# Optimization experiments

Measured on AMD Instinct MI355X. Metric: run time of the kernel, lower is better.

## Reference

```python
import jax, jax.numpy as jnp
import numpy as np

B, N, T, F_IN = 16, 1024, 12, 1
D_MODEL, D_K, D_V, H, K = 512, 32, 32, 3, 3
C = 32  # nb_chev_filter == nb_time_filter


def _ln(x, g, b, eps=1e-5):
    mu = jnp.mean(x, -1, keepdims=True)
    var = jnp.var(x, -1, keepdims=True)
    return (x - mu) * jax.lax.rsqrt(var + eps) * g + b


def _conv(x, w, b):
    y = jax.lax.conv_general_dilated(x, w, (1, 1), 'VALID',
                                     dimension_numbers=('NCHW', 'OIHW', 'NCHW'))
    return y + b[None, :, None, None]


def setup_inputs() -> dict:
    key = jax.random.key(0)
    ks = iter(jax.random.split(key, 40))
    rn = lambda s, sc=0.02: jax.random.normal(next(ks), s, jnp.float32) * sc
    return dict(
        x=rn((B, N, F_IN, T), 1.0),
        res_att=rn((B, F_IN, H, T, T), 0.1),
        pos_embed_T=rn((T, N)),
        gamma_T=jnp.ones((N,)), beta_T=jnp.zeros((N,)),
        WQ_t=rn((N, D_K * H)), WK_t=rn((N, D_K * H)), WV_t=rn((N, D_V * H)),
        fc_t=rn((H * D_V, N)),
        pre_conv_w=rn((D_MODEL, T, 1, F_IN)), pre_conv_b=rn((D_MODEL,)),
        pos_embed_S=rn((N, D_MODEL)),
        gamma_S=jnp.ones((D_MODEL,)), beta_S=jnp.zeros((D_MODEL,)),
        WQ_s=rn((D_MODEL, D_K * K)), WK_s=rn((D_MODEL, D_K * K)),
        cheb_polys=rn((K, N, N), 0.05),
        adj_pa=(jax.random.uniform(next(ks), (N, N)) < 0.01).astype(jnp.float32),
        cheb_mask=rn((K, N, N)),
        Theta=rn((K, F_IN, C), 0.1),
        gtu3_w=rn((2 * C, C, 1, 3)), gtu3_b=rn((2 * C,)),
        gtu5_w=rn((2 * C, C, 1, 5)), gtu5_b=rn((2 * C,)),
        gtu7_w=rn((2 * C, C, 1, 7)), gtu7_b=rn((2 * C,)),
        res_conv_w=rn((C, F_IN, 1, 1)), res_conv_b=rn((C,)),
        fcmy_w=rn((3 * T - 12, T)), fcmy_b=rn((T,)),
        gamma_f=jnp.ones((C,)), beta_f=jnp.zeros((C,)),
    )


def reference(x, res_att, pos_embed_T, gamma_T, beta_T, WQ_t, WK_t, WV_t, fc_t,
              pre_conv_w, pre_conv_b, pos_embed_S, gamma_S, beta_S, WQ_s, WK_s,
              cheb_polys, adj_pa, cheb_mask, Theta,
              gtu3_w, gtu3_b, gtu5_w, gtu5_b, gtu7_w, gtu7_b,
              res_conv_w, res_conv_b, fcmy_w, fcmy_b, gamma_f, beta_f):
    B_, N_, F_, T_ = x.shape
    # ---- temporal embedding (num_of_features == 1 branch): (B,F,T,N) ----
    TEmx = _ln(jnp.transpose(x, (0, 2, 3, 1)) + pos_embed_T[None, None], gamma_T, beta_T)

    # ---- temporal MHA with residual attention bias ----
    def heads(e, W, d):
        y = e @ W  # (B,F,T,H*d)
        return jnp.transpose(y.reshape(B_, F_, T_, H, d), (0, 1, 3, 2, 4))  # (B,F,H,T,d)
    Q, Kt, V = heads(TEmx, WQ_t, D_K), heads(TEmx, WK_t, D_K), heads(TEmx, WV_t, D_V)
    re_At = jnp.einsum('bfhqd,bfhkd->bfhqk', Q, Kt) / np.sqrt(D_K) + res_att
    attn = jax.nn.softmax(re_At, axis=-1)
    ctx = jnp.einsum('bfhqk,bfhkd->bfhqd', attn, V)
    ctx = jnp.transpose(ctx, (0, 1, 3, 2, 4)).reshape(B_, F_, T_, H * D_V)
    one_n, zero_n = jnp.ones((N_,), x.dtype), jnp.zeros((N_,), x.dtype)
    TATout = _ln(ctx @ fc_t + TEmx, one_n, zero_n)  # fresh LayerNorm(d_model) -> gamma=1, beta=0

    # ---- pre_conv: Conv2d(T, d_model, kernel=(1,F)) on (B,T,N,F); take last col ----
    x_TAt = jnp.einsum('btnf,dtf->bnd', jnp.transpose(TATout, (0, 2, 3, 1)),
                       pre_conv_w[:, :, 0, :]) + pre_conv_b  # (B,N,d_model)

    # ---- spatial embedding + spatial attention scores (no softmax) ----
    SEmx = _ln(x_TAt + pos_embed_S[None], gamma_S, beta_S)  # dropout = identity (eval)
    Qs = jnp.transpose((SEmx @ WQ_s).reshape(B_, N_, K, D_K), (0, 2, 1, 3))
    Ks = jnp.transpose((SEmx @ WK_s).reshape(B_, N_, K, D_K), (0, 2, 1, 3))
    STAt = jnp.einsum('bknd,bkmd->bknm', Qs, Ks) / np.sqrt(D_K)  # (B,K,N,N)

    # ---- Chebyshev graph conv weighted by spatial attention ----
    satt = jax.nn.softmax(STAt + (adj_pa[None] * cheb_mask)[None], axis=2)
    Tka = cheb_polys[None] * satt  # (B,K,N,N)
    rhs = jnp.einsum('bkmn,bmft->bknft', Tka, x)  # T_k_with_at^T @ x over all t
    spatial_gcn = jax.nn.relu(jnp.einsum('bknft,kfo->bnot', rhs, Theta))  # (B,N,C,T)

    # ---- gated temporal convs (GTU) ----
    X = jnp.transpose(spatial_gcn, (0, 2, 1, 3))  # (B,C,N,T)
    def gtu(w, b):
        y = _conv(X, w, b)
        return jnp.tanh(y[:, :C]) * jax.nn.sigmoid(y[:, C:])
    time_conv = jnp.concatenate([gtu(gtu3_w, gtu3_b), gtu(gtu5_w, gtu5_b),
                                 gtu(gtu7_w, gtu7_b)], axis=-1)  # (B,C,N,3T-12)
    time_conv = time_conv @ fcmy_w + fcmy_b  # (B,C,N,T)
    tco = jax.nn.relu(time_conv)  # num_of_features == 1 branch

    # ---- residual 1x1 conv + final LayerNorm over channel dim ----
    x_res = _conv(jnp.transpose(x, (0, 2, 1, 3)), res_conv_w, res_conv_b)  # (B,C,N,T)
    out = _ln(jnp.transpose(jax.nn.relu(x_res + tco), (0, 3, 2, 1)), gamma_f, beta_f)
    out = jnp.transpose(out, (0, 2, 3, 1))  # (B,N,C,T)
    return out, re_At
```

## Files before the change

### kernel.cpp

```cpp
#include <hip/hip_runtime.h>
#include <hip/hip_bf16.h>
#include <math.h>

#define B_ 16
#define N_ 1024
#define T_ 12
#define DM_ 512
#define H_ 3
#define K_ 3
#define C_ 32
#define RSQRT_DK 0.17677669529663687f

typedef __attribute__((ext_vector_type(8))) short bf16x8;
typedef __attribute__((ext_vector_type(4))) float f32x4;

__device__ __forceinline__ ushort f2bf(float f) {
  uint u = __float_as_uint(f);
  return (ushort)((u + 0x7FFF + ((u >> 16) & 1)) >> 16);
}

__global__ void k1_temporal_ln(const float* __restrict__ x, const float* __restrict__ posT,
                               const float* __restrict__ gT, const float* __restrict__ bT,
                               float* __restrict__ TEmx) {
  int row = blockIdx.x;
  int b = row / T_, t = row - b * T_;
  __shared__ float red[256], red2[256];
  float v[4]; float s = 0.f, s2 = 0.f;
  for (int i = 0; i < 4; ++i) {
    int n = threadIdx.x + (i << 8);
    float val = x[(b * N_ + n) * T_ + t] + posT[t * N_ + n];
    v[i] = val; s += val; s2 += val * val;
  }
  red[threadIdx.x] = s; red2[threadIdx.x] = s2;
  __syncthreads();
  for (int off = 128; off > 0; off >>= 1) {
    if (threadIdx.x < off) { red[threadIdx.x] += red[threadIdx.x + off]; red2[threadIdx.x] += red2[threadIdx.x + off]; }
    __syncthreads();
  }
  float mu = red[0] * (1.f / N_);
  float rs = rsqrtf(red2[0] * (1.f / N_) - mu * mu + 1e-5f);
  for (int i = 0; i < 4; ++i) {
    int n = threadIdx.x + (i << 8);
    TEmx[row * N_ + n] = (v[i] - mu) * rs * gT[n] + bT[n];
  }
}

__global__ __launch_bounds__(256) void k2_qkv(const float* __restrict__ TEmx,
                       const float* __restrict__ WQ, const float* __restrict__ WK,
                       const float* __restrict__ WV, float* __restrict__ part) {
  int kc = blockIdx.x, row = blockIdx.y;
  __shared__ float e[256];
  int tid = threadIdx.x;
  e[tid] = TEmx[row * N_ + kc * 256 + tid];
  __syncthreads();
  for (int col = tid; col < 288; col += 256) {
    int which = col / 96, j = col - which * 96;
    const float* W = (which == 0) ? WQ : ((which == 1) ? WK : WV);
    const float* Wp = W + (size_t)(kc * 256) * 96 + j;
    float acc = 0.f;
    #pragma unroll 8
    for (int n = 0; n < 256; ++n) acc += e[n] * Wp[n * 96];
    part[(row * 4 + kc) * 288 + col] = acc;
  }
}

__global__ void k3a_attn(const float* __restrict__ part, const float* __restrict__ res_att,
                         float* __restrict__ reAt_out, float* __restrict__ ctx) {
  int b = blockIdx.x;
  __shared__ float q_l[T_ * 288];
  __shared__ float s_l[H_ * T_ * T_];
  for (int i = threadIdx.x; i < T_ * 288; i += 256) {
    int t = i / 288, col = i - t * 288;
    const float* pr = &part[(size_t)((b * T_ + t) * 4) * 288 + col];
    q_l[i] = pr[0] + pr[288] + pr[576] + pr[864];
  }
  __syncthreads();
  for (int idx = threadIdx.x; idx < H_ * T_ * T_; idx += 256) {
    int h = idx / 144, r = idx - h * 144, qi = r / 12, ki = r - qi * 12;
    float acc = 0.f;
    #pragma unroll
    for (int d = 0; d < 32; ++d)
      acc += q_l[qi * 288 + h * 32 + d] * q_l[ki * 288 + 96 + h * 32 + d];
    float sv = acc * RSQRT_DK + res_att[(b * H_ + h) * 144 + qi * 12 + ki];
    s_l[idx] = sv;
    reAt_out[(b * H_ + h) * 144 + qi * 12 + ki] = sv;
  }
  __syncthreads();
  if (threadIdx.x < 36) {
    int h = threadIdx.x / 12, qi = threadIdx.x - h * 12;
    float mx = -1e30f;
    for (int ki = 0; ki < 12; ++ki) mx = fmaxf(mx, s_l[h * 144 + qi * 12 + ki]);
    float sum = 0.f;
    for (int ki = 0; ki < 12; ++ki) { float p = __expf(s_l[h * 144 + qi * 12 + ki] - mx); s_l[h * 144 + qi * 12 + ki] = p; sum += p; }
    float inv = 1.f / sum;
    for (int ki = 0; ki < 12; ++ki) s_l[h * 144 + qi * 12 + ki] *= inv;
  }
  __syncthreads();
  for (int idx = threadIdx.x; idx < T_ * 96; idx += 256) {
    int qi = idx / 96, hd = idx - qi * 96, h = hd >> 5, d = hd & 31;
    float acc = 0.f;
    for (int ki = 0; ki < 12; ++ki)
      acc += s_l[h * 144 + qi * 12 + ki] * q_l[ki * 288 + 192 + h * 32 + d];
    ctx[(b * T_ + qi) * 96 + hd] = acc;
  }
}

__global__ __launch_bounds__(1024) void k3b_tat(const float* __restrict__ ctx,
                        const float* __restrict__ fc_t,
                        const float* __restrict__ TEmx, float* __restrict__ TAT) {
  int row = blockIdx.x;
  __shared__ float c_l[96];
  __shared__ float red[16], red2[16];
  int tid = threadIdx.x;
  if (tid < 96) c_l[tid] = ctx[row * 96 + tid];
  __syncthreads();
  float acc = TEmx[row * N_ + tid];
  #pragma unroll 12
  for (int j = 0; j < 96; ++j) acc = fmaf(c_l[j], fc_t[j * N_ + tid], acc);
  float s = acc, s2 = acc * acc;
  #pragma unroll
  for (int off = 32; off > 0; off >>= 1) {
    s  += __shfl_xor(s, off);
    s2 += __shfl_xor(s2, off);
  }
  int w = tid >> 6;
  if ((tid & 63) == 0) { red[w] = s; red2[w] = s2; }
  __syncthreads();
  float ts = 0.f, ts2 = 0.f;
  #pragma unroll
  for (int i = 0; i < 16; ++i) { ts += red[i]; ts2 += red2[i]; }
  float mu = ts * (1.f / N_);
  float rs = rsqrtf(ts2 * (1.f / N_) - mu * mu + 1e-5f);
  TAT[row * N_ + tid] = (acc - mu) * rs;
}

__global__ void k4_preconv_ln(const float* __restrict__ TAT, const float* __restrict__ pcw,
                              const float* __restrict__ pcb, const float* __restrict__ posS,
                              const float* __restrict__ gS, const float* __restrict__ bS,
                              float* __restrict__ SEmx) {
  int bn = blockIdx.x; int b = bn >> 10, n = bn & 1023;
  __shared__ float tc[12];
  __shared__ float red[256], red2[256];
  if (threadIdx.x < 12) tc[threadIdx.x] = TAT[(b * T_ + threadIdx.x) * N_ + n];
  __syncthreads();
  float v[2]; float s = 0.f, s2 = 0.f;
  for (int i = 0; i < 2; ++i) {
    int d = threadIdx.x + (i << 8);
    float acc = pcb[d];
    #pragma unroll
    for (int t = 0; t < 12; ++t) acc += tc[t] * pcw[d * 12 + t];
    acc += posS[n * DM_ + d];
    v[i] = acc; s += acc; s2 += acc * acc;
  }
  red[threadIdx.x] = s; red2[threadIdx.x] = s2;
  __syncthreads();
  for (int off = 128; off > 0; off >>= 1) {
    if (threadIdx.x < off) { red[threadIdx.x] += red[threadIdx.x + off]; red2[threadIdx.x] += red2[threadIdx.x + off]; }
    __syncthreads();
  }
  float mu = red[0] * (1.f / DM_);
  float rs = rsqrtf(red2[0] * (1.f / DM_) - mu * mu + 1e-5f);
  for (int i = 0; i < 2; ++i) {
    int d = threadIdx.x + (i << 8);
    SEmx[bn * DM_ + d] = (v[i] - mu) * rs * gS[d] + bS[d];
  }
}

__global__ void k5_pre(const float* __restrict__ WQs, const float* __restrict__ WKs,
                       ushort* __restrict__ wpre) {
  int idx = blockIdx.x * 256 + threadIdx.x;
  int k = idx / 192, col = idx - k * 192;
  float v = (col < 96) ? WQs[k * 96 + col] : WKs[k * 96 + (col - 96)];
  wpre[col * 512 + k] = f2bf(v);
}

__global__ __launch_bounds__(256) void k5_qks(const float* __restrict__ SEmx,
                                              const ushort* __restrict__ wpre,
                                              __hip_bfloat16* __restrict__ Qs,
                                              __hip_bfloat16* __restrict__ Ks) {
  int b = blockIdx.y, n0 = blockIdx.x * 32;
  __shared__ __align__(16) ushort SE_h[32 * 520];
  int tid = threadIdx.x;
  for (int idx = tid; idx < 4096; idx += 256) {
    int r = idx >> 7, cq = idx & 127;
    float4 v = *(const float4*)&SEmx[((size_t)((b << 10) + n0 + r)) * DM_ + cq * 4];
    uint lo = (uint)f2bf(v.x) | ((uint)f2bf(v.y) << 16);
    uint hi = (uint)f2bf(v.z) | ((uint)f2bf(v.w) << 16);
    *(uint2*)&SE_h[r * 520 + cq * 4] = make_uint2(lo, hi);
  }
  __syncthreads();

  int w = tid >> 6, lane = tid & 63, quad = lane >> 4, c16 = lane & 15;
  f32x4 acc[3][2];
  #pragma unroll
  for (int mi = 0; mi < 3; ++mi)
    #pragma unroll
    for (int nt = 0; nt < 2; ++nt) acc[mi][nt] = (f32x4){0.f, 0.f, 0.f, 0.f};

  for (int ks = 0; ks < 16; ++ks) {
    bf16x8 Bf0 = *(const bf16x8*)&SE_h[(0 * 16 + c16) * 520 + ks * 32 + quad * 8];
    bf16x8 Bf1 = *(const bf16x8*)&SE_h[(1 * 16 + c16) * 520 + ks * 32 + quad * 8];
    #pragma unroll
    for (int mi = 0; mi < 3; ++mi) {
      int m = (w * 3 + mi) * 16 + c16;
      bf16x8 Af = *(const bf16x8*)&wpre[m * 512 + ks * 32 + quad * 8];
      acc[mi][0] = __builtin_amdgcn_mfma_f32_16x16x32_bf16(Af, Bf0, acc[mi][0], 0, 0, 0);
      acc[mi][1] = __builtin_amdgcn_mfma_f32_16x16x32_bf16(Af, Bf1, acc[mi][1], 0, 0, 0);
    }
  }
  #pragma unroll
  for (int mi = 0; mi < 3; ++mi) {
    int mb = (w * 3 + mi) * 16;
    #pragma unroll
    for (int nt = 0; nt < 2; ++nt) {
      int node = n0 + nt * 16 + c16;
      #pragma unroll
      for (int r = 0; r < 4; ++r) {
        int m = mb + quad * 4 + r;
        int j = (m < 96) ? m : m - 96;
        int kk = j >> 5, dd = j & 31;
        __hip_bfloat16* o = (m < 96) ? Qs : Ks;
        o[(((b * K_ + kk) * N_) + node) * 32 + dd] = __float2bfloat16(acc[mi][nt][r]);
      }
    }
  }
}

__global__ void k6_pre(const float* __restrict__ adj, const float* __restrict__ mask,
                       const float* __restrict__ cheb, uint* __restrict__ pk) {
  int idx = blockIdx.x * 256 + threadIdx.x;
  int mn = idx & (N_ * N_ - 1);
  uint lo = f2bf(adj[mn] * mask[idx]);
  uint hi = f2bf(cheb[idx]);
  pk[idx] = lo | (hi << 16);
}

__global__ __launch_bounds__(256) void k6_spatial(
    const __hip_bfloat16* __restrict__ Qs, const __hip_bfloat16* __restrict__ Ks,
    const uint* __restrict__ pk, const float* __restrict__ x,
    float* __restrict__ rhs) {
  const int b  = blockIdx.x;
  const int k  = blockIdx.y;
  const int n0 = blockIdx.z * 32;
  const ushort* Qb = (const ushort*)(Qs + (size_t)((b * K_ + k) * N_) * 32);
  const ushort* Kb = (const ushort*)(Ks + (size_t)((b * K_ + k) * N_) * 32);
  const uint* pkk = pk + (size_t)k * (N_ * N_);
  const float* xb = x + b * N_ * T_;

  __shared__ float wmu[4][32], well[4][32];
  __shared__ float wacc[4][32][12];

  const int tid  = threadIdx.x;
  const int w    = tid >> 6, lane = tid & 63;
  const int quad = lane >> 4, c16 = lane & 15;

  bf16x8 bfr0 = *(const bf16x8*)(Kb + (size_t)(n0 + c16) * 32 + quad * 8);
  bf16x8 bfr1 = *(const bf16x8*)(Kb + (size_t)(n0 + 16 + c16) * 32 + quad * 8);

  float mu0 = -1e30f, mu1 = -1e30f, el0 = 0.f, el1 = 0.f;
  float acc0[12], acc1[12];
  #pragma unroll
  for (int t = 0; t < 12; ++t) { acc0[t] = 0.f; acc1[t] = 0.f; }

  for (int s = 0; s < 16; ++s) {
    const int m0 = s * 64 + w * 16;
    bf16x8 af = *(const bf16x8*)(Qb + (size_t)(m0 + c16) * 32 + quad * 8);
    f32x4 z = {0.f, 0.f, 0.f, 0.f};
    f32x4 sc0 = __builtin_amdgcn_mfma_f32_16x16x32_bf16(af, bfr0, z, 0, 0, 0);
    f32x4 sc1 = __builtin_amdgcn_mfma_f32_16x16x32_bf16(af, bfr1, z, 0, 0, 0);

    const int mrow = m0 + quad * 4;
    float sv0[4], sv1[4], ch0[4], ch1[4];
    #pragma unroll
    for (int r = 0; r < 4; ++r) {
      uint p2 = pkk[(size_t)(mrow + r) * N_ + n0 + c16];
      uint q2 = pkk[(size_t)(mrow + r) * N_ + n0 + 16 + c16];
      sv0[r] = sc0[r] * RSQRT_DK + __uint_as_float(p2 << 16);
      ch0[r] = __uint_as_float(p2 & 0xFFFF0000u);
      sv1[r] = sc1[r] * RSQRT_DK + __uint_as_float(q2 << 16);
      ch1[r] = __uint_as_float(q2 & 0xFFFF0000u);
    }
    float cm0 = fmaxf(fmaxf(sv0[0], sv0[1]), fmaxf(sv0[2], sv0[3]));
    float cm1 = fmaxf(fmaxf(sv1[0], sv1[1]), fmaxf(sv1[2], sv1[3]));
    cm0 = fmaxf(cm0, __shfl_xor(cm0, 16)); cm0 = fmaxf(cm0, __shfl_xor(cm0, 32));
    cm1 = fmaxf(cm1, __shfl_xor(cm1, 16)); cm1 = fmaxf(cm1, __shfl_xor(cm1, 32));
    float nm0 = fmaxf(mu0, cm0), nm1 = fmaxf(mu1, cm1);
    float f0 = __expf(mu0 - nm0), f1 = __expf(mu1 - nm1);
    mu0 = nm0; mu1 = nm1;
    el0 *= f0; el1 *= f1;
    #pragma unroll
    for (int t = 0; t < 12; ++t) { acc0[t] *= f0; acc1[t] *= f1; }

    float p0[4], p1[4];
    #pragma unroll
    for (int r = 0; r < 4; ++r) {
      p0[r] = __expf(sv0[r] - mu0); el0 += p0[r]; p0[r] *= ch0[r];
      p1[r] = __expf(sv1[r] - mu1); el1 += p1[r]; p1[r] *= ch1[r];
    }
    #pragma unroll
    for (int r = 0; r < 4; ++r) {
      const float4* xr = (const float4*)(xb + (size_t)(mrow + r) * 12);
      float4 xA = xr[0], xB = xr[1], xC = xr[2];
      float xv[12] = {xA.x, xA.y, xA.z, xA.w, xB.x, xB.y, xB.z, xB.w,
                      xC.x, xC.y, xC.z, xC.w};
      float px0 = p0[r], px1 = p1[r];
      #pragma unroll
      for (int t = 0; t < 12; ++t) {
        acc0[t] = fmaf(px0, xv[t], acc0[t]);
        acc1[t] = fmaf(px1, xv[t], acc1[t]);
      }
    }
  }

  #pragma unroll
  for (int off = 16; off <= 32; off <<= 1) {
    el0 += __shfl_xor(el0, off);
    el1 += __shfl_xor(el1, off);
    #pragma unroll
    for (int t = 0; t < 12; ++t) {
      acc0[t] += __shfl_xor(acc0[t], off);
      acc1[t] += __shfl_xor(acc1[t], off);
    }
  }
  if (quad == 0) {
    wmu[w][c16] = mu0; well[w][c16] = el0;
    #pragma unroll
    for (int t = 0; t < 12; ++t) wacc[w][c16][t] = acc0[t];
  } else if (quad == 1) {
    wmu[w][16 + c16] = mu1; well[w][16 + c16] = el1;
    #pragma unroll
    for (int t = 0; t < 12; ++t) wacc[w][16 + c16][t] = acc1[t];
  }
  __syncthreads();
  if (tid < 384) {
    int n = tid / 12, t = tid - n * 12;
    float m0v = wmu[0][n], m1v = wmu[1][n], m2v = wmu[2][n], m3v = wmu[3][n];
    float gm = fmaxf(fmaxf(m0v, m1v), fmaxf(m2v, m3v));
    float e0 = __expf(m0v - gm), e1 = __expf(m1v - gm);
    float e2 = __expf(m2v - gm), e3 = __expf(m3v - gm);
    float den = well[0][n] * e0 + well[1][n] * e1 + well[2][n] * e2 + well[3][n] * e3;
    float num = wacc[0][n][t] * e0 + wacc[1][n][t] * e1 +
                wacc[2][n][t] * e2 + wacc[3][n][t] * e3;
    rhs[((size_t)(b * K_ + k) * N_ + n0 + n) * 12 + t] = num / den;
  }
}

template<int KS, int JV, int JB>
__device__ __forceinline__ void conv_mfma(const ushort* X_th, const ushort* wl_h,
                                          ushort* tc_h, const float* bias0,
                                          int mp, int ntg, int quad, int c16) {
  f32x4 accA[3], accB[3];
  #pragma unroll
  for (int i = 0; i < 3; ++i) { accA[i] = (f32x4){0.f,0.f,0.f,0.f}; accB[i] = (f32x4){0.f,0.f,0.f,0.f}; }
  #pragma unroll
  for (int dt = 0; dt < KS; ++dt) {
    bf16x8 A0 = *(const bf16x8*)&wl_h[dt * 2560 + (mp * 16 + c16) * 40 + quad * 8];
    bf16x8 A1 = *(const bf16x8*)&wl_h[dt * 2560 + ((mp + 2) * 16 + c16) * 40 + quad * 8];
    #pragma unroll
    for (int i = 0; i < 3; ++i) {
      int nt = ntg * 3 + i;
      int j = nt >> 1, sh = nt & 1;
      bf16x8 Bf = *(const bf16x8*)&X_th[(sh * 16 + c16) * 584 + (j + dt) * 32 + quad * 8];
      accA[i] = __builtin_amdgcn_mfma_f32_16x16x32_bf16(A0, Bf, accA[i], 0, 0, 0);
      accB[i] = __builtin_amdgcn_mfma_f32_16x16x32_bf16(A1, Bf, accB[i], 0, 0, 0);
    }
  }
  #pragma unroll
  for (int i = 0; i < 3; ++i) {
    int nt = ntg * 3 + i, j = nt >> 1, sh = nt & 1;
    if (j < JV) {
      int s = sh * 16 + c16;
      int sx = (s & 15) << 1;
      #pragma unroll
      for (int r = 0; r < 4; ++r) {
        int cc = mp * 16 + quad * 4 + r;
        float a = accA[i][r] + bias0[cc];
        float g = accB[i][r] + bias0[cc + 32];
        float e2a = __expf(2.f * a);
        float th = 1.f - 2.f / (e2a + 1.f);
        float sg = 1.f / (1.f + __expf(-g));
        tc_h[((s * 32 + cc) * 32 + (JB + j)) ^ sx] = f2bf(th * sg);
      }
    }
  }
}

__global__ __launch_bounds__(1024) void k8_fused(
                       const float* __restrict__ rhs, const float* __restrict__ Theta,
                       const float* __restrict__ x, const float* __restrict__ rw,
                       const float* __restrict__ rb,
                       const float* __restrict__ w3, const float* __restrict__ b3,
                       const float* __restrict__ w5, const float* __restrict__ b5,
                       const float* __restrict__ w7, const float* __restrict__ b7,
                       const float* __restrict__ fw, const float* __restrict__ fb,
                       const float* __restrict__ gf, const float* __restrict__ bf,
                       float* __restrict__ out) {
  int bn0 = blockIdx.x * 32;
  int b = bn0 >> 10, n0 = bn0 & 1023;

  __shared__ __align__(16) char uR[73216];
  ushort* X_th = (ushort*)uR;
  ushort* wl_h = (ushort*)(uR + 37376);
  float*  v_l  = (float*)uR;
  __shared__ __align__(16) ushort tc_h[1024 * 32];
  __shared__ float rhs_l[32 * 36];
  __shared__ float Th_l[96];
  __shared__ float xr_l[32 * 12];
  __shared__ float fw_l[288];
  __shared__ float fb_l[12];
  __shared__ float bias_l[3][64];
  __shared__ float rw_l[32], rb_l[32], gf_l[32], bf_l[32];
  __shared__ float stm[384], str[384];

  int tid = threadIdx.x;
  int w = tid >> 6, lane = tid & 63, quad = lane >> 4, c16 = lane & 15;
  int mp = w & 1, ntg = w >> 1;
  int c = (tid >> 3) & 31;
  int site = (tid & 7) | ((tid >> 8) << 3);

  for (int idx = tid; idx < 1152; idx += 1024) {
    int s = idx / 36, r = idx - s * 36, k = r / 12, t = r - k * 12;
    rhs_l[idx] = rhs[((size_t)(b * 3 + k) * N_ + n0 + s) * 12 + t];
  }
  if (tid < 384) xr_l[tid] = x[(size_t)(b * N_ + n0) * 12 + tid];
  if (tid < 96) Th_l[tid] = Theta[tid];
  if (tid < 288) fw_l[tid] = fw[tid];
  if (tid < 12) fb_l[tid] = fb[tid];
  if (tid < 64) { bias_l[0][tid] = b3[tid]; bias_l[1][tid] = b5[tid]; bias_l[2][tid] = b7[tid]; }
  if (tid >= 64 && tid < 96)  rw_l[tid - 64] = rw[tid - 64];
  if (tid >= 96 && tid < 128) rb_l[tid - 96] = rb[tid - 96];
  if (tid >= 128 && tid < 160) gf_l[tid - 128] = gf[tid - 128];
  if (tid >= 160 && tid < 192) bf_l[tid - 160] = bf[tid - 160];
  for (int idx = tid; idx < 64 * 32 * 3; idx += 1024) {
    int co = idx / 96, r2 = idx - co * 96, ic = r2 / 3, dt = r2 - ic * 3;
    wl_h[dt * 2560 + co * 40 + ic] = f2bf(w3[idx]);
  }
  __syncthreads();

  {
    float th0 = Th_l[c], th1 = Th_l[32 + c], th2 = Th_l[64 + c];
    const float* rs_ = &rhs_l[site * 36];
    ushort* xo = &X_th[site * 584 + c];
    #pragma unroll
    for (int t = 0; t < 12; ++t) {
      float a = rs_[t] * th0 + rs_[12 + t] * th1 + rs_[24 + t] * th2;
      xo[t * 32] = f2bf(fmaxf(a, 0.f));
    }
  }
  for (int idx = tid; idx < 32 * 6 * 32; idx += 1024) {
    int s = idx / 192, r2 = idx - s * 192, tt = r2 >> 5, ic = r2 & 31;
    X_th[s * 584 + (12 + tt) * 32 + ic] = 0;
  }
  __syncthreads();

  conv_mfma<3, 10, 0>(X_th, wl_h, tc_h, &bias_l[0][0], mp, ntg, quad, c16);
  __syncthreads();
  for (int idx = tid; idx < 64 * 32 * 5; idx += 1024) {
    int co = idx / 160, r2 = idx - co * 160, ic = r2 / 5, dt = r2 - ic * 5;
    wl_h[dt * 2560 + co * 40 + ic] = f2bf(w5[idx]);
  }
  __syncthreads();
  conv_mfma<5, 8, 10>(X_th, wl_h, tc_h, &bias_l[1][0], mp, ntg, quad, c16);
  __syncthreads();
  for (int idx = tid; idx < 64 * 32 * 7; idx += 1024) {
    int co = idx / 224, r2 = idx - co * 224, ic = r2 / 7, dt = r2 - ic * 7;
    wl_h[dt * 2560 + co * 40 + ic] = f2bf(w7[idx]);
  }
  __syncthreads();
  conv_mfma<7, 6, 18>(X_th, wl_h, tc_h, &bias_l[2][0], mp, ntg, quad, c16);
  __syncthreads();

  float tcv[24];
  {
    int rb2 = (site * 32 + c) * 32;
    int sx = (site & 15) << 1;
    #pragma unroll
    for (int j = 0; j < 24; ++j)
      tcv[j] = __uint_as_float(((uint)tc_h[(rb2 + j) ^ sx]) << 16);
  }
  float o[12];
  #pragma unroll
  for (int t = 0; t < 12; ++t) o[t] = fb_l[t];
  #pragma unroll
  for (int j = 0; j < 24; ++j) {
    const float4* fp = (const float4*)&fw_l[j * 12];
    float4 f0 = fp[0], f1 = fp[1], f2 = fp[2];
    float fr[12] = {f0.x, f0.y, f0.z, f0.w, f1.x, f1.y, f1.z, f1.w, f2.x, f2.y, f2.z, f2.w};
    #pragma unroll
    for (int t = 0; t < 12; ++t) o[t] = fmaf(tcv[j], fr[t], o[t]);
  }

  float v[12];
  {
    float rwc = rw_l[c], rbc = rb_l[c];
    const float* xs = &xr_l[site * 12];
    float* vo = &v_l[site * 391 + c * 12];
    #pragma unroll
    for (int t = 0; t < 12; ++t) {
      float xres = xs[t] * rwc + rbc;
      v[t] = fmaxf(xres + fmaxf(o[t], 0.f), 0.f);
      vo[t] = v[t];
    }
  }
  __syncthreads();
  if (tid < 384) {
    int s = tid / 12, t = tid - s * 12;
    float sm = 0.f, s2 = 0.f;
    #pragma unroll 8
    for (int cc = 0; cc < 32; ++cc) {
      float u = v_l[s * 391 + cc * 12 + t];
      sm += u; s2 += u * u;
    }
    float m = sm * (1.f / 32.f);
    stm[tid] = m;
    str[tid] = rsqrtf(s2 * (1.f / 32.f) - m * m + 1e-5f);
  }
  __syncthreads();
  {
    float gfc = gf_l[c], bfc = bf_l[c];
    const float* sm_ = &stm[site * 12];
    const float* sr_ = &str[site * 12];
    float q[12];
    #pragma unroll
    for (int t = 0; t < 12; ++t) q[t] = (v[t] - sm_[t]) * sr_[t] * gfc + bfc;
    float* op = &out[(size_t)(bn0 + site) * 384 + c * 12];
    ((float4*)op)[0] = make_float4(q[0], q[1], q[2], q[3]);
    ((float4*)op)[1] = make_float4(q[4], q[5], q[6], q[7]);
    ((float4*)op)[2] = make_float4(q[8], q[9], q[10], q[11]);
  }
}

extern "C" void kernel_launch(void* const* d_in, const int* in_sizes, int n_in,
                              void* d_out, int out_size, void* d_ws, size_t ws_size,
                              hipStream_t stream) {
  const float* x       = (const float*)d_in[0];
  const float* res_att = (const float*)d_in[1];
  const float* posT    = (const float*)d_in[2];
  const float* gT      = (const float*)d_in[3];
  const float* bT      = (const float*)d_in[4];
  const float* WQt     = (const float*)d_in[5];
  const float* WKt     = (const float*)d_in[6];
  const float* WVt     = (const float*)d_in[7];
  const float* fct     = (const float*)d_in[8];
  const float* pcw     = (const float*)d_in[9];
  const float* pcb     = (const float*)d_in[10];
  const float* posS    = (const float*)d_in[11];
  const float* gS      = (const float*)d_in[12];
  const float* bS      = (const float*)d_in[13];
  const float* WQs     = (const float*)d_in[14];
  const float* WKs     = (const float*)d_in[15];
  const float* cheb    = (const float*)d_in[16];
  const float* adj     = (const float*)d_in[17];
  const float* mask    = (const float*)d_in[18];
  const float* Theta   = (const float*)d_in[19];
  const float* w3      = (const float*)d_in[20];
  const float* b3      = (const float*)d_in[21];
  const float* w5      = (const float*)d_in[22];
  const float* b5      = (const float*)d_in[23];
  const float* w7      = (const float*)d_in[24];
  const float* b7      = (const float*)d_in[25];
  const float* rw      = (const float*)d_in[26];
  const float* rb      = (const float*)d_in[27];
  const float* fw      = (const float*)d_in[28];
  const float* fb      = (const float*)d_in[29];
  const float* gf      = (const float*)d_in[30];
  const float* bf      = (const float*)d_in[31];

  float* ws = (float*)d_ws;
  float* TEmx = ws;
  float* qkv  = TEmx + 196608;
  float* ctx  = qkv + 55296;
  float* TAT  = ctx + 18432;
  float* SEmx = TAT + 196608;
  float* Qsf  = SEmx + 8388608;
  float* Ksf  = Qsf + 1572864;
  float* rhs  = Ksf + 1572864;
  ushort* wpre = (ushort*)(rhs + 589824);
  float* part = SEmx;

  __hip_bfloat16* Qh = (__hip_bfloat16*)Qsf;
  __hip_bfloat16* Kh = (__hip_bfloat16*)Ksf;
  uint* pk = (uint*)SEmx;

  float* out  = (float*)d_out;
  float* reAt = out + 6291456;

  k5_pre<<<(DM_ * 192) / 256, 256, 0, stream>>>(WQs, WKs, wpre);
  k1_temporal_ln<<<B_ * T_, 256, 0, stream>>>(x, posT, gT, bT, TEmx);
  k2_qkv<<<dim3(4, B_ * T_), 256, 0, stream>>>(TEmx, WQt, WKt, WVt, part);
  k3a_attn<<<B_, 256, 0, stream>>>(part, res_att, reAt, ctx);
  k3b_tat<<<B_ * T_, 1024, 0, stream>>>(ctx, fct, TEmx, TAT);
  k4_preconv_ln<<<B_ * N_, 256, 0, stream>>>(TAT, pcw, pcb, posS, gS, bS, SEmx);
  k5_qks<<<dim3(N_ / 32, B_), 256, 0, stream>>>(SEmx, wpre, Qh, Kh);
  k6_pre<<<(K_ * N_ * N_) / 256, 256, 0, stream>>>(adj, mask, cheb, pk);
  k6_spatial<<<dim3(B_, K_, N_ / 32), 256, 0, stream>>>(Qh, Kh, pk, x, rhs);
  k8_fused<<<B_ * N_ / 32, 1024, 0, stream>>>(rhs, Theta, x, rw, rb,
                                              w3, b3, w5, b5, w7, b7, fw, fb, gf, bf, out);
}
```

Baseline: 351.3 us.

## Use wave-per-row LayerNorm in preconv, skip padded MFMAs, reswizzle GTU tile

The preconv+LayerNorm kernel now handles one (b,n) row per 64-lane wavefront instead of one per 256-thread block. It loads weights as float4 and reduces with shuffles rather than shared-memory tree reductions and barriers. The GTU conv MFMA loop skips tiles whose output column is out of range, avoiding wasted LDS loads and MFMAs. The XOR swizzle on the gated-conv output tile also mixes in channel bits, which is meant to reduce LDS bank conflicts on writes and reads.

```diff
diff --git a/kernel.cpp b/kernel.cpp
--- a/kernel.cpp
+++ b/kernel.cpp
@@ -17,6 +17,9 @@
 __device__ __forceinline__ ushort f2bf(float f) {
   uint u = __float_as_uint(f);
   return (ushort)((u + 0x7FFF + ((u >> 16) & 1)) >> 16);
+}
+__device__ __forceinline__ float bf2f(ushort h) {
+  return __uint_as_float(((uint)h) << 16);
 }
 
 __global__ void k1_temporal_ln(const float* __restrict__ x, const float* __restrict__ posT,
@@ -134,35 +137,40 @@
   TAT[row * N_ + tid] = (acc - mu) * rs;
 }
 
-__global__ void k4_preconv_ln(const float* __restrict__ TAT, const float* __restrict__ pcw,
+__global__ __launch_bounds__(256) void k4_preconv_ln(const float* __restrict__ TAT, const float* __restrict__ pcw,
                               const float* __restrict__ pcb, const float* __restrict__ posS,
                               const float* __restrict__ gS, const float* __restrict__ bS,
                               float* __restrict__ SEmx) {
-  int bn = blockIdx.x; int b = bn >> 10, n = bn & 1023;
-  __shared__ float tc[12];
-  __shared__ float red[256], red2[256];
-  if (threadIdx.x < 12) tc[threadIdx.x] = TAT[(b * T_ + threadIdx.x) * N_ + n];
-  __syncthreads();
-  float v[2]; float s = 0.f, s2 = 0.f;
-  for (int i = 0; i < 2; ++i) {
-    int d = threadIdx.x + (i << 8);
+  int wid = blockIdx.x * 4 + (threadIdx.x >> 6);
+  int b = wid >> 10, n = wid & 1023;
+  int lane = threadIdx.x & 63;
+  float tc[12];
+  #pragma unroll
+  for (int t = 0; t < 12; ++t) tc[t] = TAT[(b * T_ + t) * N_ + n];
+  float v[8]; float s = 0.f, s2 = 0.f;
+  #pragma unroll
+  for (int i = 0; i < 8; ++i) {
+    int d = lane + (i << 6);
+    const float4* pw = (const float4*)&pcw[d * 12];
+    float4 w0 = pw[0], w1 = pw[1], w2 = pw[2];
     float acc = pcb[d];
-    #pragma unroll
-    for (int t = 0; t < 12; ++t) acc += tc[t] * pcw[d * 12 + t];
-    acc += posS[n * DM_ + d];
+    acc += tc[0] * w0.x + tc[1] * w0.y + tc[2] * w0.z + tc[3] * w0.w;
+    acc += tc[4] * w1.x + tc[5] * w1.y + tc[6] * w1.z + tc[7] * w1.w;
+    acc += tc[8] * w2.x + tc[9] * w2.y + tc[10] * w2.z + tc[11] * w2.w;
+    acc += posS[(size_t)n * DM_ + d];
     v[i] = acc; s += acc; s2 += acc * acc;
   }
-  red[threadIdx.x] = s; red2[threadIdx.x] = s2;
-  __syncthreads();
-  for (int off = 128; off > 0; off >>= 1) {
-    if (threadIdx.x < off) { red[threadIdx.x] += red[threadIdx.x + off]; red2[threadIdx.x] += red2[threadIdx.x + off]; }
-    __syncthreads();
-  }
-  float mu = red[0] * (1.f / DM_);
-  float rs = rsqrtf(red2[0] * (1.f / DM_) - mu * mu + 1e-5f);
-  for (int i = 0; i < 2; ++i) {
-    int d = threadIdx.x + (i << 8);
-    SEmx[bn * DM_ + d] = (v[i] - mu) * rs * gS[d] + bS[d];
+  #pragma unroll
+  for (int off = 1; off < 64; off <<= 1) {
+    s  += __shfl_xor(s, off);
+    s2 += __shfl_xor(s2, off);
+  }
+  float mu = s * (1.f / DM_);
+  float rs = rsqrtf(s2 * (1.f / DM_) - mu * mu + 1e-5f);
+  #pragma unroll
+  for (int i = 0; i < 8; ++i) {
+    int d = lane + (i << 6);
+    SEmx[(size_t)wid * DM_ + d] = (v[i] - mu) * rs * gS[d] + bS[d];
   }
 }
 
@@ -360,9 +368,11 @@
     for (int i = 0; i < 3; ++i) {
       int nt = ntg * 3 + i;
       int j = nt >> 1, sh = nt & 1;
-      bf16x8 Bf = *(const bf16x8*)&X_th[(sh * 16 + c16) * 584 + (j + dt) * 32 + quad * 8];
-      accA[i] = __builtin_amdgcn_mfma_f32_16x16x32_bf16(A0, Bf, accA[i], 0, 0, 0);
-      accB[i] = __builtin_amdgcn_mfma_f32_16x16x32_bf16(A1, Bf, accB[i], 0, 0, 0);
+      if (j < JV) {
+        bf16x8 Bf = *(const bf16x8*)&X_th[(sh * 16 + c16) * 584 + (j + dt) * 32 + quad * 8];
+        accA[i] = __builtin_amdgcn_mfma_f32_16x16x32_bf16(A0, Bf, accA[i], 0, 0, 0);
+        accB[i] = __builtin_amdgcn_mfma_f32_16x16x32_bf16(A1, Bf, accB[i], 0, 0, 0);
+      }
     }
   }
   #pragma unroll
@@ -370,10 +380,10 @@
     int nt = ntg * 3 + i, j = nt >> 1, sh = nt & 1;
     if (j < JV) {
       int s = sh * 16 + c16;
-      int sx = (s & 15) << 1;
       #pragma unroll
       for (int r = 0; r < 4; ++r) {
         int cc = mp * 16 + quad * 4 + r;
+        int sx = ((s & 15) << 1) ^ ((cc & 4) << 3) ^ ((cc & 8) >> 1);
         float a = accA[i][r] + bias0[cc];
         float g = accB[i][r] + bias0[cc + 32];
         float e2a = __expf(2.f * a);
@@ -473,10 +483,10 @@
   float tcv[24];
   {
     int rb2 = (site * 32 + c) * 32;
-    int sx = (site & 15) << 1;
+    int sxr = ((site & 15) << 1) ^ ((c & 4) << 3) ^ ((c & 8) >> 1);
     #pragma unroll
     for (int j = 0; j < 24; ++j)
-      tcv[j] = __uint_as_float(((uint)tc_h[(rb2 + j) ^ sx]) << 16);
+      tcv[j] = __uint_as_float(((uint)tc_h[(rb2 + j) ^ sxr]) << 16);
   }
   float o[12];
   #pragma unroll
@@ -590,7 +600,7 @@
   k2_qkv<<<dim3(4, B_ * T_), 256, 0, stream>>>(TEmx, WQt, WKt, WVt, part);
   k3a_attn<<<B_, 256, 0, stream>>>(part, res_att, reAt, ctx);
   k3b_tat<<<B_ * T_, 1024, 0, stream>>>(ctx, fct, TEmx, TAT);
-  k4_preconv_ln<<<B_ * N_, 256, 0, stream>>>(TAT, pcw, pcb, posS, gS, bS, SEmx);
+  k4_preconv_ln<<<B_ * N_ / 4, 256, 0, stream>>>(TAT, pcw, pcb, posS, gS, bS, SEmx);
   k5_qks<<<dim3(N_ / 32, B_), 256, 0, stream>>>(SEmx, wpre, Qh, Kh);
   k6_pre<<<(K_ * N_ * N_) / 256, 256, 0, stream>>>(adj, mask, cheb, pk);
   k6_spatial<<<dim3(B_, K_, N_ / 32), 256, 0, stream>>>(Qh, Kh, pk, x, rhs);
```

New measurement: 363.7 us. +3.5%, slower.
